# Optimization experiments

Hardware: AMD Instinct MI355X
Metric: run time of the kernel (lower is better)

The kernel has to match this reference:

```python
import jax, jax.numpy as jnp
import numpy as np

B, D, NH = 32768, 32, 128
SCALE = 0.05  # weight init scale; keeps exp(s) well-conditioned


def setup_inputs() -> dict:
    key = jax.random.key(0)
    ks = jax.random.split(key, 10)
    x = jax.random.normal(ks[0], (B, D), jnp.float32)
    # layer 0: LeafParam(2) -> learned constant (s, t)
    p0 = jax.random.normal(ks[1], (2,), jnp.float32) * SCALE
    # per-dim MLPs for i = 1..D-1, stacked. Layer i consumes x[:, :i]; we pad
    # its first weight to (D, NH) with rows >= i zeroed so a single batched
    # einsum computes all per-dim nets at once (same math as the python loop).
    mask = (jnp.arange(D)[None, :] < jnp.arange(1, D)[:, None]).astype(jnp.float32)  # (D-1, D)
    W1 = jax.random.normal(ks[2], (D - 1, D, NH), jnp.float32) * SCALE * mask[:, :, None]
    b1 = jax.random.normal(ks[3], (D - 1, NH), jnp.float32) * SCALE
    W2 = jax.random.normal(ks[4], (D - 1, NH, NH), jnp.float32) * SCALE
    b2 = jax.random.normal(ks[5], (D - 1, NH), jnp.float32) * SCALE
    W3 = jax.random.normal(ks[6], (D - 1, NH, NH), jnp.float32) * SCALE
    b3 = jax.random.normal(ks[7], (D - 1, NH), jnp.float32) * SCALE
    W4 = jax.random.normal(ks[8], (D - 1, NH, 2), jnp.float32) * SCALE
    b4 = jax.random.normal(ks[9], (D - 1, 2), jnp.float32) * SCALE
    return dict(x=x, p0=p0, W1=W1, b1=b1, W2=W2, b2=b2, W3=W3, b3=b3, W4=W4, b4=b4)


def _lrelu(h):
    return jnp.where(h >= 0, h, 0.2 * h)  # LeakyReLU(0.2)


def reference(x, p0, W1, b1, W2, b2, W3, b3, W4, b4):
    # All D-1 per-dim MLPs in parallel. W1 rows >= i are zero, so
    h = _lrelu(jnp.einsum('bd,idh->bih', x, W1) + b1[None])     # (B, D-1, NH)
    h = _lrelu(jnp.einsum('bih,ihk->bik', h, W2) + b2[None])
    h = _lrelu(jnp.einsum('bih,ihk->bik', h, W3) + b3[None])
    st = jnp.einsum('bih,iho->bio', h, W4) + b4[None]           # (B, D-1, 2)
    st0 = jnp.broadcast_to(p0[None, None, :], (x.shape[0], 1, 2))
    st = jnp.concatenate([st0, st], axis=1)                     # (B, D, 2)
    s, t = st[..., 0], st[..., 1]
    z = x * jnp.exp(s) + t      # parity=True -> order is the identity permutation
    log_det = jnp.sum(s, axis=1)                                # (B,)
    return z, log_det
```

## Files before the change

### kernel.cpp

```cpp
#include <hip/hip_runtime.h>

typedef __bf16 v8bf  __attribute__((ext_vector_type(8)));
typedef float  f32x4  __attribute__((ext_vector_type(4)));
typedef float  f32x16 __attribute__((ext_vector_type(16)));
typedef unsigned int u32;
typedef u32 u32x4 __attribute__((ext_vector_type(4)));
typedef unsigned short u16;

#define NI   31
#define DD   32
#define NHID 128
#define NCHUNK 32
#define ITERS  4
#define NET_EL 36864
#define W2F_EL 4096
#define W3F_EL 20480
#define LDS_W4T 73728
#define LDS_BB  74240
#define LDS_BYTES 75008

__device__ __forceinline__ u32 cvtpk(float lo, float hi) {
    u32 r;
    asm("v_cvt_pk_bf16_f32 %0, %1, %2" : "=v"(r) : "v"(lo), "v"(hi));
    return r;
}

__device__ __forceinline__ void repack_tile(const f32x16 c, v8bf* f0, v8bf* f1) {
    f32x16 v;
    #pragma unroll
    for (int r = 0; r < 16; ++r) { float x = c[r]; v[r] = fmaxf(x, 0.2f * x); }
    #pragma unroll
    for (int p = 0; p < 2; ++p) {
        u32 a0 = cvtpk(v[8*p + 0], v[8*p + 1]);
        u32 a1 = cvtpk(v[8*p + 2], v[8*p + 3]);
        u32 b0 = cvtpk(v[8*p + 4], v[8*p + 5]);
        u32 b1 = cvtpk(v[8*p + 6], v[8*p + 7]);
        asm("v_permlane32_swap_b32 %0, %1" : "+v"(a0), "+v"(b0));
        asm("v_permlane32_swap_b32 %0, %1" : "+v"(a1), "+v"(b1));
        u32x4 wd = {a0, a1, b0, b1};
        if (p == 0) *f0 = __builtin_bit_cast(v8bf, wd);
        else        *f1 = __builtin_bit_cast(v8bf, wd);
    }
}

__global__ void maf_prep(const float* __restrict__ W1, const float* __restrict__ W2,
                         const float* __restrict__ W3, __bf16* __restrict__ blob,
                         const float* __restrict__ x, const float* __restrict__ p0,
                         float* __restrict__ zout, float* __restrict__ ldout) {
    int b = blockIdx.x, t = threadIdx.x;
    __shared__ float panel[16 * 128];
    if (b < 3 * NI) {
        int kind = b / NI, i = b % NI;
        const float* src; __bf16* dst; int NKS;
        if (kind == 0)      { src = W2 + (size_t)i * NHID * NHID; dst = blob + (size_t)i * NET_EL + W2F_EL; NKS = 8; }
        else if (kind == 1) { src = W3 + (size_t)i * NHID * NHID; dst = blob + (size_t)i * NET_EL + W3F_EL; NKS = 8; }
        else                { src = W1 + (size_t)i * DD * NHID;   dst = blob + (size_t)i * NET_EL;          NKS = 2; }
        const int fo = t & 127, hi2 = t >> 7;
        const int mt = fo >> 5, c = fo & 31;
        for (int ksb = 0; ksb < NKS; ++ksb) {
            #pragma unroll
            for (int r = 0; r < 8; ++r) {
                int e = r * 256 + t;
                panel[e] = src[(size_t)(ksb * 16 + (e >> 7)) * NHID + (e & 127)];
            }
            __syncthreads();
            __bf16 tmp[8];
            #pragma unroll
            for (int j = 0; j < 8; ++j) tmp[j] = (__bf16)panel[(hi2 * 8 + j) * 128 + fo];
            *(u32x4*)&dst[((size_t)(mt * NKS + ksb) * 64 + hi2 * 32 + c) * 8] = *(u32x4*)tmp;
            __syncthreads();
        }
    } else {
        int row = (b - 3 * NI) * 256 + t;
        float s = p0[0], tt = p0[1];
        ldout[row] = s;
        zout[(size_t)row * DD] = x[(size_t)row * DD] * expf(s) + tt;
    }
}

__global__ __launch_bounds__(256, 2) void maf_main(
    const float* __restrict__ x, const __bf16* __restrict__ blob,
    const float* __restrict__ b1, const float* __restrict__ b2,
    const float* __restrict__ b3,
    const float* __restrict__ W4, const float* __restrict__ b4,
    float* __restrict__ zout, float* __restrict__ ldout) {

    extern __shared__ __align__(16) char smem[];
    __bf16* w4t = (__bf16*)(smem + LDS_W4T);
    __bf16* bb  = (__bf16*)(smem + LDS_BB);
    const __bf16* wlds = (const __bf16*)smem;

    const int t = threadIdx.x;
    const int i = blockIdx.x / NCHUNK;
    const int chunk = blockIdx.x % NCHUNK;
    const int l = t & 63, w = t >> 6, c = l & 31, hi = l >> 5;

    {
        const u32x4* src = (const u32x4*)(blob + (size_t)i * NET_EL);
        u32x4* dst = (u32x4*)smem;
        #pragma unroll
        for (int k = 0; k < 18; ++k) dst[k * 256 + t] = src[k * 256 + t];
        w4t[t] = (__bf16)W4[(size_t)i * 2 * NHID + (t & 127) * 2 + (t >> 7)];
        if (t < NHID) {
            bb[t]       = (__bf16)b1[i * NHID + t];
            bb[128 + t] = (__bf16)b2[i * NHID + t];
            bb[256 + t] = (__bf16)b3[i * NHID + t];
        }
    }
    __syncthreads();

    const u32 ones0 = (hi == 0) ? 0x3F80u : 0u;
    const v8bf Bones = __builtin_bit_cast(v8bf, (u32x4){ones0, 0u, 0u, 0u});
    const float s0 = b4[2 * i], t0 = b4[2 * i + 1];
    const f32x16 zz = {};

    f32x16 acc[4][2];
    v8bf Bf[2][8];
    v8bf Bx[2][2];

#define LOADX(R0)                                                                     \
    { _Pragma("unroll")                                                               \
      for (int nt = 0; nt < 2; ++nt)                                                  \
          _Pragma("unroll")                                                           \
          for (int ks = 0; ks < 2; ++ks) {                                            \
              const float* xp = x + (size_t)((R0) + nt * 32 + c) * DD + ks * 16 + hi * 8; \
              f32x4 x0 = *(const f32x4*)xp;                                           \
              f32x4 x1 = *(const f32x4*)(xp + 4);                                     \
              u32x4 wd = {cvtpk(x0[0], x0[1]), cvtpk(x0[2], x0[3]),                   \
                          cvtpk(x1[0], x1[1]), cvtpk(x1[2], x1[3])};                  \
              Bx[nt][ks] = __builtin_bit_cast(v8bf, wd);                              \
          } }

#define ABIAS(BOFF, MT)                                                               \
    __builtin_bit_cast(v8bf, (u32x4){                                                 \
        (hi == 0) ? (u32)__builtin_bit_cast(u16, bb[(BOFF) + (MT) * 32 + c]) : 0u,    \
        0u, 0u, 0u})

#define HIDDEN(BASE_EL, BOFF)                                                         \
    {                                                                                 \
        _Pragma("unroll")                                                             \
        for (int mt = 0; mt < 4; ++mt) {                                              \
            v8bf Ab = ABIAS(BOFF, mt);                                                \
            acc[mt][0] = __builtin_amdgcn_mfma_f32_32x32x16_bf16(Ab, Bones, zz, 0, 0, 0); \
            acc[mt][1] = __builtin_amdgcn_mfma_f32_32x32x16_bf16(Ab, Bones, zz, 0, 0, 0); \
        }                                                                             \
        _Pragma("unroll")                                                             \
        for (int ks = 0; ks < 8; ++ks) {                                              \
            v8bf A[4];                                                                \
            _Pragma("unroll")                                                         \
            for (int mt = 0; mt < 4; ++mt)                                            \
                A[mt] = *(const v8bf*)&wlds[(BASE_EL) + ((mt * 8 + ks) * 64 + l) * 8]; \
            _Pragma("unroll")                                                         \
            for (int mt = 0; mt < 4; ++mt)                                            \
                _Pragma("unroll")                                                     \
                for (int nt = 0; nt < 2; ++nt)                                        \
                    acc[mt][nt] = __builtin_amdgcn_mfma_f32_32x32x16_bf16(            \
                        A[mt], Bf[nt][ks], acc[mt][nt], 0, 0, 0);                     \
        }                                                                             \
        _Pragma("unroll")                                                             \
        for (int mt = 0; mt < 4; ++mt)                                                \
            _Pragma("unroll")                                                         \
            for (int nt = 0; nt < 2; ++nt)                                            \
                repack_tile(acc[mt][nt], &Bf[nt][2 * mt], &Bf[nt][2 * mt + 1]);       \
    }

    LOADX(chunk * 1024 + w * 64)

    for (int it = 0; it < ITERS; ++it) {
        const int row0 = chunk * 1024 + it * 256 + w * 64;

        #pragma unroll
        for (int mt = 0; mt < 4; ++mt) {
            v8bf Ab = ABIAS(0, mt);
            v8bf A0 = *(const v8bf*)&wlds[((mt * 2 + 0) * 64 + l) * 8];
            v8bf A1 = *(const v8bf*)&wlds[((mt * 2 + 1) * 64 + l) * 8];
            #pragma unroll
            for (int nt = 0; nt < 2; ++nt) {
                f32x16 a = __builtin_amdgcn_mfma_f32_32x32x16_bf16(Ab, Bones, zz, 0, 0, 0);
                a = __builtin_amdgcn_mfma_f32_32x32x16_bf16(A0, Bx[nt][0], a, 0, 0, 0);
                a = __builtin_amdgcn_mfma_f32_32x32x16_bf16(A1, Bx[nt][1], a, 0, 0, 0);
                acc[mt][nt] = a;
            }
        }
        #pragma unroll
        for (int mt = 0; mt < 4; ++mt)
            #pragma unroll
            for (int nt = 0; nt < 2; ++nt)
                repack_tile(acc[mt][nt], &Bf[nt][2 * mt], &Bf[nt][2 * mt + 1]);

        HIDDEN(W2F_EL, 128)
        HIDDEN(W3F_EL, 256)

        if (it + 1 < ITERS) LOADX(chunk * 1024 + (it + 1) * 256 + w * 64)

        {
            f32x16 acc4[2];
            acc4[0] = zz; acc4[1] = zz;
            #pragma unroll
            for (int ks = 0; ks < 8; ++ks) {
                v8bf a4 = {};
                if (c < 2) a4 = *(const v8bf*)&w4t[c * NHID + ks * 16 + hi * 8];
                acc4[0] = __builtin_amdgcn_mfma_f32_32x32x16_bf16(a4, Bf[0][ks], acc4[0], 0, 0, 0);
                acc4[1] = __builtin_amdgcn_mfma_f32_32x32x16_bf16(a4, Bf[1][ks], acc4[1], 0, 0, 0);
            }
            if (hi == 0) {
                #pragma unroll
                for (int nt = 0; nt < 2; ++nt) {
                    int row = row0 + nt * 32 + c;
                    float s  = acc4[nt][0] + s0;
                    float tt = acc4[nt][1] + t0;
                    float xv = x[(size_t)row * DD + i + 1];
                    zout[(size_t)row * DD + i + 1] = xv * expf(s) + tt;
                    atomicAdd(&ldout[row], s);
                }
            }
        }
    }
#undef LOADX
#undef ABIAS
#undef HIDDEN
}

extern "C" void kernel_launch(void* const* d_in, const int* in_sizes, int n_in,
                              void* d_out, int out_size, void* d_ws, size_t ws_size,
                              hipStream_t stream) {
    (void)in_sizes; (void)n_in; (void)out_size; (void)ws_size;
    const float* x  = (const float*)d_in[0];
    const float* p0 = (const float*)d_in[1];
    const float* W1 = (const float*)d_in[2];
    const float* b1 = (const float*)d_in[3];
    const float* W2 = (const float*)d_in[4];
    const float* b2 = (const float*)d_in[5];
    const float* W3 = (const float*)d_in[6];
    const float* b3 = (const float*)d_in[7];
    const float* W4 = (const float*)d_in[8];
    const float* b4 = (const float*)d_in[9];

    float* zout  = (float*)d_out;
    float* ldout = zout + (size_t)32768 * DD;

    __bf16* blob = (__bf16*)d_ws;

    hipFuncSetAttribute((const void*)maf_main,
                        hipFuncAttributeMaxDynamicSharedMemorySize, LDS_BYTES);

    maf_prep<<<3 * NI + 128, 256, 0, stream>>>(W1, W2, W3, blob, x, p0, zout, ldout);
    maf_main<<<NI * NCHUNK, 256, LDS_BYTES, stream>>>(x, blob, b1, b2, b3, W4, b4,
                                                      zout, ldout);
}
```

Before: 109.7 us.

## Prepack x into bf16 MFMA fragments and transposed copy in prep kernel

The prep kernel now converts x once into bf16 MFMA B-fragment layout and also writes a transposed fp32 copy, so the main kernel loads ready-made fragments instead of converting fp32 rows per network. Networks with index below 16 skip the second K-step of layer 1, because their W1 rows past 16 are zero. The next-iteration x load is moved earlier to overlap with the hidden layers, and the final x read becomes coalesced through xT. This adds extra workspace traffic and more work in the prep kernel.

```diff
diff --git a/kernel.cpp b/kernel.cpp
--- a/kernel.cpp
+++ b/kernel.cpp
@@ -10,6 +10,7 @@
 #define NI   31
 #define DD   32
 #define NHID 128
+#define NROW 32768
 #define NCHUNK 32
 #define ITERS  4
 #define NET_EL 36864
@@ -45,11 +46,12 @@
 
 __global__ void maf_prep(const float* __restrict__ W1, const float* __restrict__ W2,
                          const float* __restrict__ W3, __bf16* __restrict__ blob,
+                         __bf16* __restrict__ xfrag, float* __restrict__ xT,
                          const float* __restrict__ x, const float* __restrict__ p0,
                          float* __restrict__ zout, float* __restrict__ ldout) {
     int b = blockIdx.x, t = threadIdx.x;
-    __shared__ float panel[16 * 128];
     if (b < 3 * NI) {
+        __shared__ float panel[16 * 128];
         int kind = b / NI, i = b % NI;
         const float* src; __bf16* dst; int NKS;
         if (kind == 0)      { src = W2 + (size_t)i * NHID * NHID; dst = blob + (size_t)i * NET_EL + W2F_EL; NKS = 8; }
@@ -71,15 +73,48 @@
             __syncthreads();
         }
     } else {
-        int row = (b - 3 * NI) * 256 + t;
-        float s = p0[0], tt = p0[1];
-        ldout[row] = s;
-        zout[(size_t)row * DD] = x[(size_t)row * DD] * expf(s) + tt;
+        __shared__ float pan[64 * 33];
+        const int xb = b - 3 * NI;
+        const float s0 = p0[0], t0 = p0[1];
+        const float es = expf(s0);
+        for (int pass = 0; pass < 4; ++pass) {
+            const int rb = xb * 256 + pass * 64;
+            #pragma unroll
+            for (int r = 0; r < 8; ++r) {
+                int e = r * 256 + t;
+                pan[(e >> 5) * 33 + (e & 31)] = x[(size_t)(rb + (e >> 5)) * DD + (e & 31)];
+            }
+            __syncthreads();
+            {
+                int row = t & 63, dbase = (t >> 6) * 8;
+                #pragma unroll
+                for (int dd = 0; dd < 8; ++dd)
+                    xT[(size_t)(dbase + dd) * NROW + rb + row] = pan[row * 33 + dbase + dd];
+            }
+            {
+                int w2 = t >> 6, l = t & 63;
+                int nt = w2 >> 1, ks = w2 & 1;
+                int c = l & 31, hi = l >> 5;
+                const float* pr = &pan[(nt * 32 + c) * 33 + ks * 16 + hi * 8];
+                f32x4 x0 = *(const f32x4*)pr;
+                f32x4 x1 = *(const f32x4*)(pr + 4);
+                u32x4 wd = {cvtpk(x0[0], x0[1]), cvtpk(x0[2], x0[3]),
+                            cvtpk(x1[0], x1[1]), cvtpk(x1[2], x1[3])};
+                *(u32x4*)&xfrag[(size_t)(rb >> 6) * 2048 + ((w2 * 64 + l) << 3)] = wd;
+            }
+            if (t < 64) {
+                int row = rb + t;
+                ldout[row] = s0;
+                zout[(size_t)row * DD] = pan[t * 33] * es + t0;
+            }
+            __syncthreads();
+        }
     }
 }
 
 __global__ __launch_bounds__(256, 2) void maf_main(
-    const float* __restrict__ x, const __bf16* __restrict__ blob,
+    const __bf16* __restrict__ xfrag, const float* __restrict__ xT,
+    const __bf16* __restrict__ blob,
     const float* __restrict__ b1, const float* __restrict__ b2,
     const float* __restrict__ b3,
     const float* __restrict__ W4, const float* __restrict__ b4,
@@ -94,6 +129,7 @@
     const int i = blockIdx.x / NCHUNK;
     const int chunk = blockIdx.x % NCHUNK;
     const int l = t & 63, w = t >> 6, c = l & 31, hi = l >> 5;
+    const bool full_k1 = (i >= 16);
 
     {
         const u32x4* src = (const u32x4*)(blob + (size_t)i * NET_EL);
@@ -118,18 +154,12 @@
     v8bf Bf[2][8];
     v8bf Bx[2][2];
 
-#define LOADX(R0)                                                                     \
-    { _Pragma("unroll")                                                               \
-      for (int nt = 0; nt < 2; ++nt)                                                  \
-          _Pragma("unroll")                                                           \
-          for (int ks = 0; ks < 2; ++ks) {                                            \
-              const float* xp = x + (size_t)((R0) + nt * 32 + c) * DD + ks * 16 + hi * 8; \
-              f32x4 x0 = *(const f32x4*)xp;                                           \
-              f32x4 x1 = *(const f32x4*)(xp + 4);                                     \
-              u32x4 wd = {cvtpk(x0[0], x0[1]), cvtpk(x0[2], x0[3]),                   \
-                          cvtpk(x1[0], x1[1]), cvtpk(x1[2], x1[3])};                  \
-              Bx[nt][ks] = __builtin_bit_cast(v8bf, wd);                              \
-          } }
+#define LOADX(G)                                                                      \
+    { const __bf16* xg = xfrag + (size_t)(G) * 2048;                                  \
+      Bx[0][0] = *(const v8bf*)&xg[(0 * 64 + l) << 3];                                \
+      if (full_k1) Bx[0][1] = *(const v8bf*)&xg[(1 * 64 + l) << 3];                   \
+      Bx[1][0] = *(const v8bf*)&xg[(2 * 64 + l) << 3];                                \
+      if (full_k1) Bx[1][1] = *(const v8bf*)&xg[(3 * 64 + l) << 3]; }
 
 #define ABIAS(BOFF, MT)                                                               \
     __builtin_bit_cast(v8bf, (u32x4){                                                 \
@@ -164,7 +194,7 @@
                 repack_tile(acc[mt][nt], &Bf[nt][2 * mt], &Bf[nt][2 * mt + 1]);       \
     }
 
-    LOADX(chunk * 1024 + w * 64)
+    LOADX((chunk * 1024 + w * 64) >> 6)
 
     for (int it = 0; it < ITERS; ++it) {
         const int row0 = chunk * 1024 + it * 256 + w * 64;
@@ -173,12 +203,14 @@
         for (int mt = 0; mt < 4; ++mt) {
             v8bf Ab = ABIAS(0, mt);
             v8bf A0 = *(const v8bf*)&wlds[((mt * 2 + 0) * 64 + l) * 8];
-            v8bf A1 = *(const v8bf*)&wlds[((mt * 2 + 1) * 64 + l) * 8];
+            v8bf A1;
+            if (full_k1) A1 = *(const v8bf*)&wlds[((mt * 2 + 1) * 64 + l) * 8];
             #pragma unroll
             for (int nt = 0; nt < 2; ++nt) {
                 f32x16 a = __builtin_amdgcn_mfma_f32_32x32x16_bf16(Ab, Bones, zz, 0, 0, 0);
                 a = __builtin_amdgcn_mfma_f32_32x32x16_bf16(A0, Bx[nt][0], a, 0, 0, 0);
-                a = __builtin_amdgcn_mfma_f32_32x32x16_bf16(A1, Bx[nt][1], a, 0, 0, 0);
+                if (full_k1)
+                    a = __builtin_amdgcn_mfma_f32_32x32x16_bf16(A1, Bx[nt][1], a, 0, 0, 0);
                 acc[mt][nt] = a;
             }
         }
@@ -188,10 +220,11 @@
             for (int nt = 0; nt < 2; ++nt)
                 repack_tile(acc[mt][nt], &Bf[nt][2 * mt], &Bf[nt][2 * mt + 1]);
 
+        if (it + 1 < ITERS)
+            LOADX((chunk * 1024 + (it + 1) * 256 + w * 64) >> 6)
+
         HIDDEN(W2F_EL, 128)
         HIDDEN(W3F_EL, 256)
-
-        if (it + 1 < ITERS) LOADX(chunk * 1024 + (it + 1) * 256 + w * 64)
 
         {
             f32x16 acc4[2];
@@ -209,7 +242,7 @@
                     int row = row0 + nt * 32 + c;
                     float s  = acc4[nt][0] + s0;
                     float tt = acc4[nt][1] + t0;
-                    float xv = x[(size_t)row * DD + i + 1];
+                    float xv = xT[(size_t)(i + 1) * NROW + row];
                     zout[(size_t)row * DD + i + 1] = xv * expf(s) + tt;
                     atomicAdd(&ldout[row], s);
                 }
@@ -237,14 +270,17 @@
     const float* b4 = (const float*)d_in[9];
 
     float* zout  = (float*)d_out;
-    float* ldout = zout + (size_t)32768 * DD;
-
-    __bf16* blob = (__bf16*)d_ws;
+    float* ldout = zout + (size_t)NROW * DD;
+
+    __bf16* blob  = (__bf16*)d_ws;
+    __bf16* xfrag = blob + (size_t)NI * NET_EL;
+    float*  xT    = (float*)(xfrag + (size_t)NROW * DD);
 
     hipFuncSetAttribute((const void*)maf_main,
                         hipFuncAttributeMaxDynamicSharedMemorySize, LDS_BYTES);
 
-    maf_prep<<<3 * NI + 128, 256, 0, stream>>>(W1, W2, W3, blob, x, p0, zout, ldout);
-    maf_main<<<NI * NCHUNK, 256, LDS_BYTES, stream>>>(x, blob, b1, b2, b3, W4, b4,
-                                                      zout, ldout);
-}
+    maf_prep<<<3 * NI + 128, 256, 0, stream>>>(W1, W2, W3, blob, xfrag, xT,
+                                               x, p0, zout, ldout);
+    maf_main<<<NI * NCHUNK, 256, LDS_BYTES, stream>>>(xfrag, xT, blob,
+                                                      b1, b2, b3, W4, b4, zout, ldout);
+}
```

Result: faster. 98.69 us (-10.0%).
